# Optimization experiments

Measured on AMD Instinct MI355X. Metric: run time of the kernel, lower is better.

The kernel has to match this reference:

```python
import jax, jax.numpy as jnp
import numpy as np

N_NODES = 20000
N_EDGES = 120000
N_GRAPHS = 512
F_IN = 300
NHID = 256
NHID_FF = 256
NOUT = 768
SLOPE = 0.2
EPS = 1e-16


def _p(key, shape, scale=0.05):
    return jax.random.normal(key, shape, dtype=jnp.float32) * scale


def setup_inputs() -> dict:
    key = jax.random.key(0)
    ks = jax.random.split(key, 24)
    inp = {
        "x": jax.random.normal(ks[0], (N_NODES, F_IN), dtype=jnp.float32),
        "edge_index": jax.random.randint(ks[1], (2, N_EDGES), 0, N_NODES, dtype=jnp.int64) if False else jax.random.randint(ks[1], (2, N_EDGES), 0, N_NODES).astype(jnp.int32),
        "batch": jnp.sort(jax.random.randint(ks[2], (N_NODES,), 0, N_GRAPHS)).astype(jnp.int32),
        # conv1: in=300 -> heads=4, C=256, concat
        "c1_wl": _p(ks[3], (4 * NHID, F_IN)),
        "c1_wr": _p(ks[4], (4 * NHID, F_IN)),
        "c1_att": _p(ks[5], (4, NHID)),
        "c1_b": jnp.zeros((4 * NHID,), jnp.float32),
        # conv2: in=1024 -> heads=4, C=256, concat
        "c2_wl": _p(ks[6], (4 * NHID, 4 * NHID)),
        "c2_wr": _p(ks[7], (4 * NHID, 4 * NHID)),
        "c2_att": _p(ks[8], (4, NHID)),
        "c2_b": jnp.zeros((4 * NHID,), jnp.float32),
        # conv3: in=1024 -> heads=6, C=256, mean (concat=False)
        "c3_wl": _p(ks[9], (6 * NHID_FF, 4 * NHID)),
        "c3_wr": _p(ks[10], (6 * NHID_FF, 4 * NHID)),
        "c3_att": _p(ks[11], (6, NHID_FF)),
        "c3_b": jnp.zeros((NHID_FF,), jnp.float32),
        # post-process MLP
        "fp1_w": _p(ks[12], (NHID_FF, NHID_FF)),
        "fp1_b": jnp.zeros((NHID_FF,), jnp.float32),
        "fp2_w": _p(ks[13], (NOUT, NHID_FF)),
        "fp2_b": jnp.zeros((NOUT,), jnp.float32),
    }
    return inp


def gatv2(x, src, dst, wl, wr, att, b, concat):
    """GATv2Conv (PyG semantics, eval mode): lin_l on source, lin_r on target,
    score = att . leaky_relu(xl_j + xr_i), segment softmax over dst, aggregate xl_j."""
    n = x.shape[0]
    H, C = att.shape
    xl = (x @ wl.T).reshape(n, H, C)
    xr = (x @ wr.T).reshape(n, H, C)
    s = xl[src] + xr[dst]                                   # [E,H,C] gather
    s = jnp.where(s > 0, s, SLOPE * s)                      # leaky_relu
    scores = jnp.einsum("ehc,hc->eh", s, att)               # [E,H]
    mx = jax.ops.segment_max(scores, dst, num_segments=n)   # [N,H]
    ex = jnp.exp(scores - mx[dst])
    denom = jax.ops.segment_sum(ex, dst, num_segments=n)
    alpha = ex / (denom[dst] + EPS)                         # [E,H]
    out = jax.ops.segment_sum(alpha[:, :, None] * xl[src], dst, num_segments=n)  # [N,H,C]
    out = out.reshape(n, H * C) if concat else out.mean(axis=1)
    return out + b


def reference(x, edge_index, batch, c1_wl, c1_wr, c1_att, c1_b,
              c2_wl, c2_wr, c2_att, c2_b, c3_wl, c3_wr, c3_att, c3_b,
              fp1_w, fp1_b, fp2_w, fp2_b):
    n = x.shape[0]
    # PyG GATv2Conv defaults add_self_loops=True
    loops = jnp.arange(n, dtype=edge_index.dtype)
    src = jnp.concatenate([edge_index[0], loops])
    dst = jnp.concatenate([edge_index[1], loops])

    h = jax.nn.elu(gatv2(x, src, dst, c1_wl, c1_wr, c1_att, c1_b, concat=True))
    h = jax.nn.elu(gatv2(h, src, dst, c2_wl, c2_wr, c2_att, c2_b, concat=True))
    h = gatv2(h, src, dst, c3_wl, c3_wr, c3_att, c3_b, concat=False)

    # F.normalize(p=2, dim=-1), torch eps=1e-12
    norm = jnp.linalg.norm(h, axis=-1, keepdims=True)
    h = h / jnp.maximum(norm, 1e-12)

    # global_mean_pool over `batch`
    sums = jax.ops.segment_sum(h, batch, num_segments=N_GRAPHS)
    cnts = jax.ops.segment_sum(jnp.ones((n,), h.dtype), batch, num_segments=N_GRAPHS)
    pooled = sums / jnp.maximum(cnts, 1.0)[:, None]

    h = jax.nn.relu(pooled @ fp1_w.T + fp1_b)
    return h @ fp2_w.T + fp2_b
```

## Files before the change

### kernel.cpp

```cpp
#include <hip/hip_runtime.h>

typedef _Float16 h16;
typedef _Float16 h16x2 __attribute__((ext_vector_type(2)));
typedef _Float16 h16x4 __attribute__((ext_vector_type(4)));
typedef _Float16 h16x8 __attribute__((ext_vector_type(8)));
typedef float f32x4 __attribute__((ext_vector_type(4)));

static constexpr int NN   = 20000;
static constexpr int NPAD = 20224;
static constexpr int NE0  = 120000;
static constexpr int NE   = 140000;
static constexpr int NG   = 512;
static constexpr int FIN  = 300;
static constexpr int K1P  = 384;
static constexpr int CD   = 256;
static constexpr float SLOPE = 0.2f;

#define GLDS16(gsrc, ldst)                                                              \
  __builtin_amdgcn_global_load_lds(                                                    \
      (const __attribute__((address_space(1))) unsigned int*)(gsrc),                    \
      (__attribute__((address_space(3))) unsigned int*)(ldst), 16, 0, 0)

__global__ __launch_bounds__(256) void fill_x_kernel(const float* __restrict__ x, h16* __restrict__ a1) {
  int r = blockIdx.x;
  for (int c = threadIdx.x; c < K1P; c += 256) {
    float v = (r < NN && c < FIN) ? x[(size_t)r * FIN + c] : 0.f;
    a1[(size_t)r * K1P + c] = (h16)v;
  }
}

__global__ __launch_bounds__(256) void conv_w2_kernel(const float* __restrict__ wl, const float* __restrict__ wr,
                                                      h16* __restrict__ o, int rows, int cols, int colsp) {
  int r = blockIdx.x;
  const float* s = (r < rows) ? (wl + (size_t)r * cols) : (wr + (size_t)(r - rows) * cols);
  for (int c = threadIdx.x; c < colsp; c += 256) {
    float v = (c < cols) ? s[c] : 0.f;
    o[(size_t)r * colsp + c] = (h16)v;
  }
}

__global__ __launch_bounds__(256) void attcvt_kernel(const float* __restrict__ a, h16* __restrict__ o, int n) {
  int i = blockIdx.x * 256 + threadIdx.x;
  if (i < n) o[i] = (h16)a[i];
}

__global__ __launch_bounds__(256) void build_edges_kernel(const int* __restrict__ ei,
                                                          int* __restrict__ src, int* __restrict__ dst) {
  int e = blockIdx.x * 256 + threadIdx.x;
  if (e >= NE) return;
  if (e < NE0) { src[e] = ei[e]; dst[e] = ei[NE0 + e]; }
  else         { src[e] = e - NE0; dst[e] = e - NE0; }
}

__global__ __launch_bounds__(256) void deg_kernel(const int* __restrict__ dst, int* __restrict__ deg) {
  int e = blockIdx.x * 256 + threadIdx.x;
  if (e < NE) atomicAdd(&deg[dst[e]], 1);
}

__global__ __launch_bounds__(1024) void scan_kernel(const int* __restrict__ deg, int* __restrict__ rowptr) {
  __shared__ int b0[1024], b1[1024];
  __shared__ int carry;
  int t = threadIdx.x;
  if (t == 0) carry = 0;
  __syncthreads();
  for (int base = 0; base < NN; base += 1024) {
    int x = (base + t < NN) ? deg[base + t] : 0;
    b0[t] = x;
    __syncthreads();
    int* cur = b0; int* nxt = b1;
    for (int off = 1; off < 1024; off <<= 1) {
      int v = cur[t];
      if (t >= off) v += cur[t - off];
      nxt[t] = v;
      __syncthreads();
      int* tmp = cur; cur = nxt; nxt = tmp;
    }
    if (base + t < NN) rowptr[base + t] = carry + cur[t] - x;
    __syncthreads();
    if (t == 0) carry += cur[1023];
    __syncthreads();
  }
  if (t == 0) rowptr[NN] = carry;
}

__global__ __launch_bounds__(256) void scatter_kernel(const int* __restrict__ src, const int* __restrict__ dst,
                                                      const int* __restrict__ rowptr, int* __restrict__ cursor,
                                                      int* __restrict__ esrc) {
  int e = blockIdx.x * 256 + threadIdx.x;
  if (e >= NE) return;
  int d = dst[e];
  int pos = rowptr[d] + atomicAdd(&cursor[d], 1);
  esrc[pos] = src[e];
}

__global__ __launch_bounds__(512, 2) void gemm256_kernel(const h16* __restrict__ A, const h16* __restrict__ B,
                                                         h16* __restrict__ Co, int K, int Nw, int ntN) {
  __shared__ __align__(16) h16 lds[4 * 16384];
  int nwg = gridDim.x;
  int q = nwg >> 3, r = nwg & 7;
  int xc = blockIdx.x & 7, idx = blockIdx.x >> 3;
  int logical = (xc < r ? xc * (q + 1) : r * (q + 1) + (xc - r) * q) + idx;
  int tm = (logical / ntN) * 256, tn = (logical % ntN) * 256;

  int tid = threadIdx.x;
  int wv = tid >> 6, lane = tid & 63;
  int wm = (wv >> 2) * 128, wn = (wv & 3) * 64;
  int lrow = lane & 15, kq = lane >> 4, lr7 = lrow & 7;

  int rowoff = tid >> 3;
  int ug = ((tid & 7) ^ (rowoff & 7)) * 8;
  int ldsoff = (tid >> 6) * 512;

  const int NT = K >> 6;

  auto STAGE = [&](int buf, int kt) {
#pragma unroll
    for (int j = 0; j < 4; ++j) {
      GLDS16(A + (size_t)(tm + j * 64 + rowoff) * K + kt * 64 + ug,
             &lds[(buf * 2 + 0) * 16384 + j * 4096 + ldsoff]);
      GLDS16(B + (size_t)(tn + j * 64 + rowoff) * K + kt * 64 + ug,
             &lds[(buf * 2 + 1) * 16384 + j * 4096 + ldsoff]);
    }
  };

  STAGE(0, 0);
  STAGE(1, 1);

  f32x4 acc[8][4] = {};
  for (int t = 0; t < NT; ++t) {
    int b = t & 1;
    if (t + 1 < NT) { asm volatile("s_waitcnt vmcnt(8)" ::: "memory"); }
    else            { asm volatile("s_waitcnt vmcnt(0)" ::: "memory"); }
    __builtin_amdgcn_s_barrier();

    const h16* As_ = &lds[(b * 2 + 0) * 16384];
    const h16* Bs_ = &lds[(b * 2 + 1) * 16384];
    h16x8 af[8], bf[4];
#pragma unroll
    for (int i = 0; i < 8; ++i) af[i] = *(const h16x8*)&As_[(wm + i * 16 + lrow) * 64 + ((kq ^ lr7) * 8)];
#pragma unroll
    for (int j = 0; j < 4; ++j) bf[j] = *(const h16x8*)&Bs_[(wn + j * 16 + lrow) * 64 + ((kq ^ lr7) * 8)];
#pragma unroll
    for (int i = 0; i < 8; ++i)
#pragma unroll
      for (int j = 0; j < 4; ++j)
        acc[i][j] = __builtin_amdgcn_mfma_f32_16x16x32_f16(af[i], bf[j], acc[i][j], 0, 0, 0);
#pragma unroll
    for (int i = 0; i < 8; ++i) af[i] = *(const h16x8*)&As_[(wm + i * 16 + lrow) * 64 + (((4 + kq) ^ lr7) * 8)];
#pragma unroll
    for (int j = 0; j < 4; ++j) bf[j] = *(const h16x8*)&Bs_[(wn + j * 16 + lrow) * 64 + (((4 + kq) ^ lr7) * 8)];
    asm volatile("s_waitcnt lgkmcnt(0)" ::: "memory");
    __builtin_amdgcn_sched_barrier(0);
    __builtin_amdgcn_s_barrier();
    if (t + 2 < NT) STAGE(b, t + 2);
    __builtin_amdgcn_s_setprio(1);
#pragma unroll
    for (int i = 0; i < 8; ++i)
#pragma unroll
      for (int j = 0; j < 4; ++j)
        acc[i][j] = __builtin_amdgcn_mfma_f32_16x16x32_f16(af[i], bf[j], acc[i][j], 0, 0, 0);
    __builtin_amdgcn_s_setprio(0);
  }

  int cr = kq * 4, cc = lrow;
#pragma unroll
  for (int i = 0; i < 8; ++i)
#pragma unroll
    for (int j = 0; j < 4; ++j) {
      size_t base = (size_t)(tm + wm + i * 16 + cr) * Nw + (tn + wn + j * 16 + cc);
#pragma unroll
      for (int qq = 0; qq < 4; qq++) Co[base + (size_t)qq * Nw] = (h16)acc[i][j][qq];
    }
}

template <int H, int MODE>
__global__ __launch_bounds__(64 * H) void sagg_kernel(
    const h16* __restrict__ X, const int* __restrict__ rowptr, const int* __restrict__ esrc,
    const h16* __restrict__ attH, const float* __restrict__ bias,
    h16* __restrict__ outA, const int* __restrict__ batch,
    float* __restrict__ pooled, int* __restrict__ cnt) {
  constexpr int HC = H * CD, S = 2 * HC;
  int n = blockIdx.x;
  int tid = threadIdx.x, w = tid >> 6, lane = tid & 63;
  int cb = w * CD + lane * 4;

  h16x4 aw4 = *(const h16x4*)(attH + cb);
  h16x2 alo = __builtin_shufflevector(aw4, aw4, 0, 1);
  h16x2 ahi = __builtin_shufflevector(aw4, aw4, 2, 3);
  h16x4 xr4 = *(const h16x4*)(X + (size_t)n * S + HC + cb);

  int beg = rowptr[n], end = rowptr[n + 1];
  float m = -1e30f, s = 0.f;
  f32x4 a = {};
  int i = beg;
  while (i < end) {
    int cn = end - i; if (cn > 8) cn = 8;
    int js[8];
    h16x4 xs[8];
    float ps[8];
#pragma unroll
    for (int k = 0; k < 8; ++k) js[k] = esrc[i + (k < cn ? k : cn - 1)];
#pragma unroll
    for (int k = 0; k < 8; ++k) xs[k] = *(const h16x4*)(X + (size_t)js[k] * S + cb);
#pragma unroll
    for (int k = 0; k < 8; ++k) {
      h16x4 v = xs[k] + xr4;
      h16x4 t = v * (h16)SLOPE;
      v = __builtin_elementwise_max(v, t);
      float p = __builtin_amdgcn_fdot2(__builtin_shufflevector(v, v, 0, 1), alo,
                __builtin_amdgcn_fdot2(__builtin_shufflevector(v, v, 2, 3), ahi, 0.f, false), false);
      p += __shfl_xor(p, 32); p += __shfl_xor(p, 16); p += __shfl_xor(p, 8);
      p += __shfl_xor(p, 4);  p += __shfl_xor(p, 2);  p += __shfl_xor(p, 1);
      ps[k] = p;
    }
#pragma unroll
    for (int k = 0; k < 8; ++k) {
      if (k < cn) {
        float p = ps[k];
        if (p <= m) {
          float we = __expf(p - m);
          s += we;
          a[0] += we * (float)xs[k][0]; a[1] += we * (float)xs[k][1];
          a[2] += we * (float)xs[k][2]; a[3] += we * (float)xs[k][3];
        } else {
          float f = __expf(m - p);
          s = s * f + 1.f;
          a[0] = a[0] * f + (float)xs[k][0]; a[1] = a[1] * f + (float)xs[k][1];
          a[2] = a[2] * f + (float)xs[k][2]; a[3] = a[3] * f + (float)xs[k][3];
          m = p;
        }
      }
    }
    i += cn;
  }
  float inv = 1.f / (s + 1e-16f);

  if (MODE == 0) {
    float o0 = a[0] * inv + bias[cb + 0];
    float o1 = a[1] * inv + bias[cb + 1];
    float o2 = a[2] * inv + bias[cb + 2];
    float o3 = a[3] * inv + bias[cb + 3];
    o0 = o0 > 0.f ? o0 : expm1f(o0);
    o1 = o1 > 0.f ? o1 : expm1f(o1);
    o2 = o2 > 0.f ? o2 : expm1f(o2);
    o3 = o3 > 0.f ? o3 : expm1f(o3);
    h16x4 ov = {(h16)o0, (h16)o1, (h16)o2, (h16)o3};
    *(h16x4*)(outA + (size_t)n * HC + cb) = ov;
  } else {
    __shared__ float sh[HC];
    __shared__ float red[H];
    float4 nv = {a[0] * inv, a[1] * inv, a[2] * inv, a[3] * inv};
    *(float4*)&sh[cb] = nv;
    __syncthreads();
    float mv = 0.f;
    if (tid < CD) {
#pragma unroll
      for (int h = 0; h < H; h++) mv += sh[h * CD + tid];
      mv = mv * (1.f / H) + bias[tid];
    }
    float ss = (tid < CD) ? mv * mv : 0.f;
    ss += __shfl_xor(ss, 32); ss += __shfl_xor(ss, 16); ss += __shfl_xor(ss, 8);
    ss += __shfl_xor(ss, 4);  ss += __shfl_xor(ss, 2);  ss += __shfl_xor(ss, 1);
    if (lane == 0) red[w] = ss;
    __syncthreads();
    float tot = 0.f;
#pragma unroll
    for (int h = 0; h < H; h++) tot += red[h];
    float scale = 1.f / fmaxf(sqrtf(tot), 1e-12f);
    int g = batch[n];
    if (tid < CD) atomicAdd(&pooled[(size_t)g * CD + tid], mv * scale);
    if (tid == 0) atomicAdd(&cnt[g], 1);
  }
}

__global__ __launch_bounds__(256) void pool_div_kernel(float* __restrict__ pooled, const int* __restrict__ cnt) {
  int g = blockIdx.x, t = threadIdx.x;
  pooled[(size_t)g * CD + t] /= fmaxf((float)cnt[g], 1.f);
}

__global__ __launch_bounds__(256) void mlp1_kernel(const float* __restrict__ pooled, const float* __restrict__ w,
                                                   const float* __restrict__ b, float* __restrict__ hid) {
  __shared__ float xs[CD];
  int g = blockIdx.x, t = threadIdx.x;
  xs[t] = pooled[(size_t)g * CD + t];
  __syncthreads();
  float acc = b[t];
  for (int k = 0; k < CD; ++k) acc += xs[k] * w[(size_t)t * CD + k];
  hid[(size_t)g * CD + t] = fmaxf(acc, 0.f);
}

__global__ __launch_bounds__(256) void mlp2_kernel(const float* __restrict__ hid, const float* __restrict__ w,
                                                   const float* __restrict__ b, float* __restrict__ out) {
  __shared__ float xs[CD];
  int g = blockIdx.x, t = threadIdx.x;
  xs[t] = hid[(size_t)g * CD + t];
  __syncthreads();
  for (int o = t; o < 768; o += 256) {
    float acc = b[o];
    for (int k = 0; k < CD; ++k) acc += xs[k] * w[(size_t)o * CD + k];
    out[(size_t)g * 768 + o] = acc;
  }
}

extern "C" void kernel_launch(void* const* d_in, const int* in_sizes, int n_in,
                              void* d_out, int out_size, void* d_ws, size_t ws_size,
                              hipStream_t stream) {
  const float* x      = (const float*)d_in[0];
  const int*   ei     = (const int*)d_in[1];
  const int*   batch  = (const int*)d_in[2];
  const float* c1_wl  = (const float*)d_in[3];
  const float* c1_wr  = (const float*)d_in[4];
  const float* c1_att = (const float*)d_in[5];
  const float* c1_b   = (const float*)d_in[6];
  const float* c2_wl  = (const float*)d_in[7];
  const float* c2_wr  = (const float*)d_in[8];
  const float* c2_att = (const float*)d_in[9];
  const float* c2_b   = (const float*)d_in[10];
  const float* c3_wl  = (const float*)d_in[11];
  const float* c3_wr  = (const float*)d_in[12];
  const float* c3_att = (const float*)d_in[13];
  const float* c3_b   = (const float*)d_in[14];
  const float* fp1_w  = (const float*)d_in[15];
  const float* fp1_b  = (const float*)d_in[16];
  const float* fp2_w  = (const float*)d_in[17];
  const float* fp2_b  = (const float*)d_in[18];

  char* p = (char*)d_ws;
  size_t off = 0;
  auto alloc = [&](size_t b) { void* r = p + off; off += (b + 255) & ~(size_t)255; return r; };
  h16*  A    = (h16*)alloc((size_t)NPAD * 1024 * 2);
  h16*  Xa   = (h16*)alloc((size_t)NPAD * 3072 * 2);
  h16*  Xb   = (h16*)alloc((size_t)NPAD * 2048 * 2);
  h16*  A1   = Xb;
  h16*  W1   = (h16*)alloc((size_t)2048 * K1P * 2);
  h16*  W2   = (h16*)alloc((size_t)2048 * 1024 * 2);
  h16*  W3   = (h16*)alloc((size_t)3072 * 1024 * 2);
  h16*  attH1 = (h16*)alloc((size_t)4 * CD * 2);
  h16*  attH2 = (h16*)alloc((size_t)4 * CD * 2);
  h16*  attH3 = (h16*)alloc((size_t)6 * CD * 2);
  int*  srcA   = (int*)alloc((size_t)NE * 4);
  int*  dstA   = (int*)alloc((size_t)NE * 4);
  int*  esrc   = (int*)alloc((size_t)NE * 4);
  int*  deg    = (int*)alloc((size_t)NN * 4);
  int*  cursor = (int*)alloc((size_t)NN * 4);
  int*  rowptr = (int*)alloc((size_t)(NN + 1) * 4);
  float* pooled = (float*)alloc((size_t)NG * CD * 4);
  int*  cnt    = (int*)alloc((size_t)NG * 4);
  float* hid   = (float*)alloc((size_t)NG * CD * 4);

  hipMemsetAsync(deg, 0, (size_t)NN * 4, stream);
  hipMemsetAsync(cursor, 0, (size_t)NN * 4, stream);
  hipMemsetAsync(pooled, 0, (size_t)NG * CD * 4, stream);
  hipMemsetAsync(cnt, 0, (size_t)NG * 4, stream);

  fill_x_kernel<<<NPAD, 256, 0, stream>>>(x, A1);
  conv_w2_kernel<<<2048, 256, 0, stream>>>(c1_wl, c1_wr, W1, 1024, FIN, K1P);
  conv_w2_kernel<<<2048, 256, 0, stream>>>(c2_wl, c2_wr, W2, 1024, 1024, 1024);
  conv_w2_kernel<<<3072, 256, 0, stream>>>(c3_wl, c3_wr, W3, 1536, 1024, 1024);
  attcvt_kernel<<<4, 256, 0, stream>>>(c1_att, attH1, 4 * CD);
  attcvt_kernel<<<4, 256, 0, stream>>>(c2_att, attH2, 4 * CD);
  attcvt_kernel<<<6, 256, 0, stream>>>(c3_att, attH3, 6 * CD);

  int eb = (NE + 255) / 256;
  build_edges_kernel<<<eb, 256, 0, stream>>>(ei, srcA, dstA);
  deg_kernel<<<eb, 256, 0, stream>>>(dstA, deg);
  scan_kernel<<<1, 1024, 0, stream>>>(deg, rowptr);
  scatter_kernel<<<eb, 256, 0, stream>>>(srcA, dstA, rowptr, cursor, esrc);

  gemm256_kernel<<<79 * 8, 512, 0, stream>>>(A1, W1, Xa, K1P, 2048, 8);
  sagg_kernel<4, 0><<<NN, 256, 0, stream>>>(Xa, rowptr, esrc, attH1, c1_b, A, nullptr, nullptr, nullptr);

  gemm256_kernel<<<79 * 8, 512, 0, stream>>>(A, W2, Xb, 1024, 2048, 8);
  sagg_kernel<4, 0><<<NN, 256, 0, stream>>>(Xb, rowptr, esrc, attH2, c2_b, A, nullptr, nullptr, nullptr);

  gemm256_kernel<<<79 * 12, 512, 0, stream>>>(A, W3, Xa, 1024, 3072, 12);
  sagg_kernel<6, 1><<<NN, 384, 0, stream>>>(Xa, rowptr, esrc, attH3, c3_b, nullptr, batch, pooled, cnt);

  pool_div_kernel<<<NG, 256, 0, stream>>>(pooled, cnt);
  mlp1_kernel<<<NG, 256, 0, stream>>>(pooled, fp1_w, fp1_b, hid);
  mlp2_kernel<<<NG, 256, 0, stream>>>(hid, fp2_w, fp2_b, (float*)d_out);
}
```

Measured before the change: 701.7 us.

## Remap GATv2 aggregation to one wavefront per node with 16-byte head-pair loads

The segment-softmax aggregation kernel now assigns one 64-lane wavefront per destination node, four nodes per block, instead of one block per node with a wave per head. Each wave loops over head pairs, loading 8 halfs per lane and reducing each score over 32 lanes. The online softmax is batched per group of 8 edges with a single rescale instead of per-edge branching. The mean-over-heads path drops shared memory and block syncs in favour of shuffles. This is meant to raise load width, cut per-node block overhead and improve occupancy, at the cost of walking each node's edge list and index loads once per head pair.

Result: slower. 810.0 us (+15.4%).

```diff
diff --git a/kernel.cpp b/kernel.cpp
--- a/kernel.cpp
+++ b/kernel.cpp
@@ -174,102 +174,127 @@
 }
 
 template <int H, int MODE>
-__global__ __launch_bounds__(64 * H) void sagg_kernel(
+__global__ __launch_bounds__(256) void sagg_kernel(
     const h16* __restrict__ X, const int* __restrict__ rowptr, const int* __restrict__ esrc,
     const h16* __restrict__ attH, const float* __restrict__ bias,
     h16* __restrict__ outA, const int* __restrict__ batch,
     float* __restrict__ pooled, int* __restrict__ cnt) {
-  constexpr int HC = H * CD, S = 2 * HC;
-  int n = blockIdx.x;
-  int tid = threadIdx.x, w = tid >> 6, lane = tid & 63;
-  int cb = w * CD + lane * 4;
-
-  h16x4 aw4 = *(const h16x4*)(attH + cb);
-  h16x2 alo = __builtin_shufflevector(aw4, aw4, 0, 1);
-  h16x2 ahi = __builtin_shufflevector(aw4, aw4, 2, 3);
-  h16x4 xr4 = *(const h16x4*)(X + (size_t)n * S + HC + cb);
-
+  constexpr int NS = H / 2;
+  constexpr int HC = H * CD;
+  constexpr unsigned ROWB = (unsigned)(4 * HC);
+  int n = blockIdx.x * 4 + (threadIdx.x >> 6);
+  if (n >= NN) return;
+  int lane = threadIdx.x & 63;
+  unsigned lby = (unsigned)lane * 16u;
+  const char* Xb = (const char*)X;
+  unsigned nrow = (unsigned)n * ROWB;
   int beg = rowptr[n], end = rowptr[n + 1];
-  float m = -1e30f, s = 0.f;
-  f32x4 a = {};
-  int i = beg;
-  while (i < end) {
-    int cn = end - i; if (cn > 8) cn = 8;
-    int js[8];
-    h16x4 xs[8];
-    float ps[8];
-#pragma unroll
-    for (int k = 0; k < 8; ++k) js[k] = esrc[i + (k < cn ? k : cn - 1)];
-#pragma unroll
-    for (int k = 0; k < 8; ++k) xs[k] = *(const h16x4*)(X + (size_t)js[k] * S + cb);
-#pragma unroll
-    for (int k = 0; k < 8; ++k) {
-      h16x4 v = xs[k] + xr4;
-      h16x4 t = v * (h16)SLOPE;
-      v = __builtin_elementwise_max(v, t);
-      float p = __builtin_amdgcn_fdot2(__builtin_shufflevector(v, v, 0, 1), alo,
-                __builtin_amdgcn_fdot2(__builtin_shufflevector(v, v, 2, 3), ahi, 0.f, false), false);
-      p += __shfl_xor(p, 32); p += __shfl_xor(p, 16); p += __shfl_xor(p, 8);
-      p += __shfl_xor(p, 4);  p += __shfl_xor(p, 2);  p += __shfl_xor(p, 1);
-      ps[k] = p;
-    }
-#pragma unroll
-    for (int k = 0; k < 8; ++k) {
-      if (k < cn) {
-        float p = ps[k];
-        if (p <= m) {
-          float we = __expf(p - m);
-          s += we;
-          a[0] += we * (float)xs[k][0]; a[1] += we * (float)xs[k][1];
-          a[2] += we * (float)xs[k][2]; a[3] += we * (float)xs[k][3];
-        } else {
-          float f = __expf(m - p);
-          s = s * f + 1.f;
-          a[0] = a[0] * f + (float)xs[k][0]; a[1] = a[1] * f + (float)xs[k][1];
-          a[2] = a[2] * f + (float)xs[k][2]; a[3] = a[3] * f + (float)xs[k][3];
-          m = p;
-        }
+
+  float t8[8];
+  if (MODE == 1) {
+#pragma unroll
+    for (int j = 0; j < 8; ++j) t8[j] = 0.f;
+  }
+
+  for (int s = 0; s < NS; ++s) {
+    unsigned sby = (unsigned)s * 1024u + lby;
+    h16x8 xr8 = *(const h16x8*)(Xb + nrow + (unsigned)(2 * HC) + sby);
+    h16x8 aw8 = *(const h16x8*)((const char*)attH + sby);
+    float m = -1e30f, den = 0.f;
+    float acc[8] = {0.f, 0.f, 0.f, 0.f, 0.f, 0.f, 0.f, 0.f};
+
+    for (int i = beg; i < end; i += 8) {
+      int cn = end - i; if (cn > 8) cn = 8;
+      unsigned offs[8];
+#pragma unroll
+      for (int k = 0; k < 8; ++k) {
+        int idx = i + k; if (idx > end - 1) idx = end - 1;
+        offs[k] = (unsigned)esrc[idx] * ROWB + sby;
       }
-    }
-    i += cn;
-  }
-  float inv = 1.f / (s + 1e-16f);
-
-  if (MODE == 0) {
-    float o0 = a[0] * inv + bias[cb + 0];
-    float o1 = a[1] * inv + bias[cb + 1];
-    float o2 = a[2] * inv + bias[cb + 2];
-    float o3 = a[3] * inv + bias[cb + 3];
-    o0 = o0 > 0.f ? o0 : expm1f(o0);
-    o1 = o1 > 0.f ? o1 : expm1f(o1);
-    o2 = o2 > 0.f ? o2 : expm1f(o2);
-    o3 = o3 > 0.f ? o3 : expm1f(o3);
-    h16x4 ov = {(h16)o0, (h16)o1, (h16)o2, (h16)o3};
-    *(h16x4*)(outA + (size_t)n * HC + cb) = ov;
-  } else {
-    __shared__ float sh[HC];
-    __shared__ float red[H];
-    float4 nv = {a[0] * inv, a[1] * inv, a[2] * inv, a[3] * inv};
-    *(float4*)&sh[cb] = nv;
-    __syncthreads();
-    float mv = 0.f;
-    if (tid < CD) {
-#pragma unroll
-      for (int h = 0; h < H; h++) mv += sh[h * CD + tid];
-      mv = mv * (1.f / H) + bias[tid];
-    }
-    float ss = (tid < CD) ? mv * mv : 0.f;
-    ss += __shfl_xor(ss, 32); ss += __shfl_xor(ss, 16); ss += __shfl_xor(ss, 8);
-    ss += __shfl_xor(ss, 4);  ss += __shfl_xor(ss, 2);  ss += __shfl_xor(ss, 1);
-    if (lane == 0) red[w] = ss;
-    __syncthreads();
-    float tot = 0.f;
-#pragma unroll
-    for (int h = 0; h < H; h++) tot += red[h];
-    float scale = 1.f / fmaxf(sqrtf(tot), 1e-12f);
+      h16x8 xv[8];
+#pragma unroll
+      for (int k = 0; k < 8; ++k) xv[k] = *(const h16x8*)(Xb + offs[k]);
+      float ps[8];
+#pragma unroll
+      for (int k = 0; k < 8; ++k) {
+        h16x8 v = xv[k] + xr8;
+        h16x8 u = v * (h16)SLOPE;
+        v = __builtin_elementwise_max(v, u);
+        float p = 0.f;
+        p = __builtin_amdgcn_fdot2(__builtin_shufflevector(v, v, 0, 1),
+                                   __builtin_shufflevector(aw8, aw8, 0, 1), p, false);
+        p = __builtin_amdgcn_fdot2(__builtin_shufflevector(v, v, 2, 3),
+                                   __builtin_shufflevector(aw8, aw8, 2, 3), p, false);
+        p = __builtin_amdgcn_fdot2(__builtin_shufflevector(v, v, 4, 5),
+                                   __builtin_shufflevector(aw8, aw8, 4, 5), p, false);
+        p = __builtin_amdgcn_fdot2(__builtin_shufflevector(v, v, 6, 7),
+                                   __builtin_shufflevector(aw8, aw8, 6, 7), p, false);
+        p += __shfl_xor(p, 1);  p += __shfl_xor(p, 2);  p += __shfl_xor(p, 4);
+        p += __shfl_xor(p, 8);  p += __shfl_xor(p, 16);
+        ps[k] = p;
+      }
+      float pm = ps[0];
+#pragma unroll
+      for (int k = 1; k < 8; ++k) pm = fmaxf(pm, ps[k]);
+      float nm = fmaxf(m, pm);
+      float f = __expf(m - nm);
+      den *= f;
+#pragma unroll
+      for (int j = 0; j < 8; ++j) acc[j] *= f;
+#pragma unroll
+      for (int k = 0; k < 8; ++k) {
+        float we = (k < cn) ? __expf(ps[k] - nm) : 0.f;
+        den += we;
+#pragma unroll
+        for (int j = 0; j < 8; ++j) acc[j] += we * (float)xv[k][j];
+      }
+      m = nm;
+    }
+    float inv = 1.f / (den + 1e-16f);
+
+    if (MODE == 0) {
+      const float* bp = bias + s * 512 + lane * 8;
+      float4 b0 = *(const float4*)bp;
+      float4 b1 = *(const float4*)(bp + 4);
+      const float* bb = (const float*)&b0;
+      const float* bb2 = (const float*)&b1;
+      h16x8 ov;
+#pragma unroll
+      for (int j = 0; j < 8; ++j) {
+        float o = acc[j] * inv + (j < 4 ? bb[j] : bb2[j - 4]);
+        o = o > 0.f ? o : expm1f(o);
+        ov[j] = (h16)o;
+      }
+      *(h16x8*)(outA + (unsigned)n * HC + s * 512 + lane * 8) = ov;
+    } else {
+#pragma unroll
+      for (int j = 0; j < 8; ++j) t8[j] += acc[j] * inv;
+    }
+  }
+
+  if (MODE == 1) {
+#pragma unroll
+    for (int j = 0; j < 8; ++j) t8[j] += __shfl_xor(t8[j], 32);
+    int cc = (lane & 31) * 8;
+    float4 b0 = *(const float4*)(bias + cc);
+    float4 b1 = *(const float4*)(bias + cc + 4);
+    const float* bb = (const float*)&b0;
+    const float* bb2 = (const float*)&b1;
+    float ss = 0.f;
+#pragma unroll
+    for (int j = 0; j < 8; ++j) {
+      t8[j] = t8[j] * (1.f / H) + (j < 4 ? bb[j] : bb2[j - 4]);
+      ss += t8[j] * t8[j];
+    }
+    ss += __shfl_xor(ss, 1);  ss += __shfl_xor(ss, 2);  ss += __shfl_xor(ss, 4);
+    ss += __shfl_xor(ss, 8);  ss += __shfl_xor(ss, 16);
+    float scale = 1.f / fmaxf(sqrtf(ss), 1e-12f);
     int g = batch[n];
-    if (tid < CD) atomicAdd(&pooled[(size_t)g * CD + tid], mv * scale);
-    if (tid == 0) atomicAdd(&cnt[g], 1);
+    if (lane < 32) {
+#pragma unroll
+      for (int j = 0; j < 8; ++j) atomicAdd(&pooled[(unsigned)g * CD + cc + j], t8[j] * scale);
+    }
+    if (lane == 0) atomicAdd(&cnt[g], 1);
   }
 }
 
@@ -367,14 +392,16 @@
   scan_kernel<<<1, 1024, 0, stream>>>(deg, rowptr);
   scatter_kernel<<<eb, 256, 0, stream>>>(srcA, dstA, rowptr, cursor, esrc);
 
+  int sb = (NN + 3) / 4;
+
   gemm256_kernel<<<79 * 8, 512, 0, stream>>>(A1, W1, Xa, K1P, 2048, 8);
-  sagg_kernel<4, 0><<<NN, 256, 0, stream>>>(Xa, rowptr, esrc, attH1, c1_b, A, nullptr, nullptr, nullptr);
+  sagg_kernel<4, 0><<<sb, 256, 0, stream>>>(Xa, rowptr, esrc, attH1, c1_b, A, nullptr, nullptr, nullptr);
 
   gemm256_kernel<<<79 * 8, 512, 0, stream>>>(A, W2, Xb, 1024, 2048, 8);
-  sagg_kernel<4, 0><<<NN, 256, 0, stream>>>(Xb, rowptr, esrc, attH2, c2_b, A, nullptr, nullptr, nullptr);
+  sagg_kernel<4, 0><<<sb, 256, 0, stream>>>(Xb, rowptr, esrc, attH2, c2_b, A, nullptr, nullptr, nullptr);
 
   gemm256_kernel<<<79 * 12, 512, 0, stream>>>(A, W3, Xa, 1024, 3072, 12);
-  sagg_kernel<6, 1><<<NN, 384, 0, stream>>>(Xa, rowptr, esrc, attH3, c3_b, nullptr, batch, pooled, cnt);
+  sagg_kernel<6, 1><<<sb, 256, 0, stream>>>(Xa, rowptr, esrc, attH3, c3_b, nullptr, batch, pooled, cnt);
 
   pool_div_kernel<<<NG, 256, 0, stream>>>(pooled, cnt);
   mlp1_kernel<<<NG, 256, 0, stream>>>(pooled, fp1_w, fp1_b, hid);
```

## Shrink GEMM tile to 256x128 with 4 waves and K-step 32, M-fastest tile order

Applied to the files above, without the earlier changes.

Restructures the GEMM from 256x256 tiles with 8 waves and a 64-wide K step to 256x128 tiles with 4 waves and a 32-wide K step. LDS use drops and the swizzle is adapted to the narrower rows. Tiles are now ordered M-fastest, so consecutive workgroups share the same weight column block. The aim is more workgroups for better occupancy and load balance across CUs, at the cost of a higher load-to-MFMA ratio per tile and more barriers per unit of work.

Measured after the change: 760.7 us. 8.4% more time.

```diff
diff --git a/kernel.cpp b/kernel.cpp
--- a/kernel.cpp
+++ b/kernel.cpp
@@ -21,6 +21,8 @@
       (const __attribute__((address_space(1))) unsigned int*)(gsrc),                    \
       (__attribute__((address_space(3))) unsigned int*)(ldst), 16, 0, 0)
 
+#define MFMA16(a, b, c) __builtin_amdgcn_mfma_f32_16x16x32_f16(a, b, c, 0, 0, 0)
+
 __global__ __launch_bounds__(256) void fill_x_kernel(const float* __restrict__ x, h16* __restrict__ a1) {
   int r = blockIdx.x;
   for (int c = threadIdx.x; c < K1P; c += 256) {
@@ -93,34 +95,35 @@
   esrc[pos] = src[e];
 }
 
-__global__ __launch_bounds__(512, 2) void gemm256_kernel(const h16* __restrict__ A, const h16* __restrict__ B,
-                                                         h16* __restrict__ Co, int K, int Nw, int ntN) {
-  __shared__ __align__(16) h16 lds[4 * 16384];
+__global__ __launch_bounds__(256, 2) void gemm256_kernel(const h16* __restrict__ A, const h16* __restrict__ B,
+                                                         h16* __restrict__ Co, int K, int Nw, int ntM) {
+  __shared__ __align__(16) h16 lds[2 * 12288];
   int nwg = gridDim.x;
   int q = nwg >> 3, r = nwg & 7;
   int xc = blockIdx.x & 7, idx = blockIdx.x >> 3;
   int logical = (xc < r ? xc * (q + 1) : r * (q + 1) + (xc - r) * q) + idx;
-  int tm = (logical / ntN) * 256, tn = (logical % ntN) * 256;
+  int tm = (logical % ntM) * 256, tn = (logical / ntM) * 128;
 
   int tid = threadIdx.x;
   int wv = tid >> 6, lane = tid & 63;
-  int wm = (wv >> 2) * 128, wn = (wv & 3) * 64;
-  int lrow = lane & 15, kq = lane >> 4, lr7 = lrow & 7;
-
-  int rowoff = tid >> 3;
-  int ug = ((tid & 7) ^ (rowoff & 7)) * 8;
-  int ldsoff = (tid >> 6) * 512;
-
-  const int NT = K >> 6;
+  int wm = (wv >> 1) * 128, wn = (wv & 1) * 64;
+  int lrow = lane & 15, kq = lane >> 4;
+  int u = (kq ^ (lrow & 3)) * 8;
+
+  int srow = tid >> 2;
+  int ug = ((tid & 3) ^ (srow & 3)) * 8;
+
+  const int NT = K >> 5;
 
   auto STAGE = [&](int buf, int kt) {
 #pragma unroll
-    for (int j = 0; j < 4; ++j) {
-      GLDS16(A + (size_t)(tm + j * 64 + rowoff) * K + kt * 64 + ug,
-             &lds[(buf * 2 + 0) * 16384 + j * 4096 + ldsoff]);
-      GLDS16(B + (size_t)(tn + j * 64 + rowoff) * K + kt * 64 + ug,
-             &lds[(buf * 2 + 1) * 16384 + j * 4096 + ldsoff]);
-    }
+    for (int j = 0; j < 4; ++j)
+      GLDS16(A + (size_t)(tm + j * 64 + srow) * K + kt * 32 + ug,
+             &lds[buf * 12288 + j * 2048 + tid * 8]);
+#pragma unroll
+    for (int j = 0; j < 2; ++j)
+      GLDS16(B + (size_t)(tn + j * 64 + srow) * K + kt * 32 + ug,
+             &lds[buf * 12288 + 8192 + j * 2048 + tid * 8]);
   };
 
   STAGE(0, 0);
@@ -129,26 +132,17 @@
   f32x4 acc[8][4] = {};
   for (int t = 0; t < NT; ++t) {
     int b = t & 1;
-    if (t + 1 < NT) { asm volatile("s_waitcnt vmcnt(8)" ::: "memory"); }
+    if (t + 1 < NT) { asm volatile("s_waitcnt vmcnt(6)" ::: "memory"); }
     else            { asm volatile("s_waitcnt vmcnt(0)" ::: "memory"); }
     __builtin_amdgcn_s_barrier();
 
-    const h16* As_ = &lds[(b * 2 + 0) * 16384];
-    const h16* Bs_ = &lds[(b * 2 + 1) * 16384];
+    const h16* As_ = &lds[b * 12288];
+    const h16* Bs_ = &lds[b * 12288 + 8192];
     h16x8 af[8], bf[4];
 #pragma unroll
-    for (int i = 0; i < 8; ++i) af[i] = *(const h16x8*)&As_[(wm + i * 16 + lrow) * 64 + ((kq ^ lr7) * 8)];
-#pragma unroll
-    for (int j = 0; j < 4; ++j) bf[j] = *(const h16x8*)&Bs_[(wn + j * 16 + lrow) * 64 + ((kq ^ lr7) * 8)];
-#pragma unroll
-    for (int i = 0; i < 8; ++i)
-#pragma unroll
-      for (int j = 0; j < 4; ++j)
-        acc[i][j] = __builtin_amdgcn_mfma_f32_16x16x32_f16(af[i], bf[j], acc[i][j], 0, 0, 0);
-#pragma unroll
-    for (int i = 0; i < 8; ++i) af[i] = *(const h16x8*)&As_[(wm + i * 16 + lrow) * 64 + (((4 + kq) ^ lr7) * 8)];
-#pragma unroll
-    for (int j = 0; j < 4; ++j) bf[j] = *(const h16x8*)&Bs_[(wn + j * 16 + lrow) * 64 + (((4 + kq) ^ lr7) * 8)];
+    for (int i = 0; i < 8; ++i) af[i] = *(const h16x8*)&As_[(wm + i * 16 + lrow) * 32 + u];
+#pragma unroll
+    for (int j = 0; j < 4; ++j) bf[j] = *(const h16x8*)&Bs_[(wn + j * 16 + lrow) * 32 + u];
     asm volatile("s_waitcnt lgkmcnt(0)" ::: "memory");
     __builtin_amdgcn_sched_barrier(0);
     __builtin_amdgcn_s_barrier();
@@ -158,7 +152,7 @@
     for (int i = 0; i < 8; ++i)
 #pragma unroll
       for (int j = 0; j < 4; ++j)
-        acc[i][j] = __builtin_amdgcn_mfma_f32_16x16x32_f16(af[i], bf[j], acc[i][j], 0, 0, 0);
+        acc[i][j] = MFMA16(af[i], bf[j], acc[i][j]);
     __builtin_amdgcn_s_setprio(0);
   }
 
@@ -367,13 +361,13 @@
   scan_kernel<<<1, 1024, 0, stream>>>(deg, rowptr);
   scatter_kernel<<<eb, 256, 0, stream>>>(srcA, dstA, rowptr, cursor, esrc);
 
-  gemm256_kernel<<<79 * 8, 512, 0, stream>>>(A1, W1, Xa, K1P, 2048, 8);
+  gemm256_kernel<<<79 * 16, 256, 0, stream>>>(A1, W1, Xa, K1P, 2048, 79);
   sagg_kernel<4, 0><<<NN, 256, 0, stream>>>(Xa, rowptr, esrc, attH1, c1_b, A, nullptr, nullptr, nullptr);
 
-  gemm256_kernel<<<79 * 8, 512, 0, stream>>>(A, W2, Xb, 1024, 2048, 8);
+  gemm256_kernel<<<79 * 16, 256, 0, stream>>>(A, W2, Xb, 1024, 2048, 79);
   sagg_kernel<4, 0><<<NN, 256, 0, stream>>>(Xb, rowptr, esrc, attH2, c2_b, A, nullptr, nullptr, nullptr);
 
-  gemm256_kernel<<<79 * 12, 512, 0, stream>>>(A, W3, Xa, 1024, 3072, 12);
+  gemm256_kernel<<<79 * 24, 256, 0, stream>>>(A, W3, Xa, 1024, 3072, 79);
   sagg_kernel<6, 1><<<NN, 384, 0, stream>>>(Xa, rowptr, esrc, attH3, c3_b, nullptr, batch, pooled, cnt);
 
   pool_div_kernel<<<NG, 256, 0, stream>>>(pooled, cnt);
```
